# Kernel optimization log

Measured on AMD Instinct MI355X. Metric: run time of the kernel, lower is better.

Reference implementation:

```python
import jax, jax.numpy as jnp
from jax import lax
import numpy as np

H = 64  # hiddenSize
I = 9   # inputSize

def _init_lstm_params(key, in_dim, hidden):
    k = 1.0 / np.sqrt(hidden)
    ks = jax.random.split(key, 4)
    w_ih = jax.random.uniform(ks[0], (4 * hidden, in_dim), minval=-k, maxval=k, dtype=jnp.float32)
    w_hh = jax.random.uniform(ks[1], (4 * hidden, hidden), minval=-k, maxval=k, dtype=jnp.float32)
    b_ih = jax.random.uniform(ks[2], (4 * hidden,), minval=-k, maxval=k, dtype=jnp.float32)
    b_hh = jax.random.uniform(ks[3], (4 * hidden,), minval=-k, maxval=k, dtype=jnp.float32)
    return w_ih, w_hh, b_ih, b_hh

def setup_inputs() -> dict:
    key = jax.random.key(0)
    kx, k0, k1, kl = jax.random.split(key, 4)
    x = jax.random.normal(kx, (4096, 336, I), dtype=jnp.float32)
    w_ih0, w_hh0, b_ih0, b_hh0 = _init_lstm_params(k0, I, H)
    w_ih1, w_hh1, b_ih1, b_hh1 = _init_lstm_params(k1, H, H)
    klw, klb = jax.random.split(kl)
    k = 1.0 / np.sqrt(H)
    w_lin = jax.random.uniform(klw, (1, H), minval=-k, maxval=k, dtype=jnp.float32)
    b_lin = jax.random.uniform(klb, (1,), minval=-k, maxval=k, dtype=jnp.float32)
    return {"x": x, "w_ih0": w_ih0, "w_hh0": w_hh0, "b_ih0": b_ih0, "b_hh0": b_hh0,
            "w_ih1": w_ih1, "w_hh1": w_hh1, "b_ih1": b_ih1, "b_hh1": b_hh1,
            "w_lin": w_lin, "b_lin": b_lin}

def _lstm_layer(x_seq, w_ih, w_hh, b_ih, b_hh):
    # x_seq: [B, T, D] -> hidden sequence [B, T, H]. PyTorch gate order: i, f, g, o.
    B = x_seq.shape[0]
    hidden = w_hh.shape[1]
    # Precompute input contribution for all timesteps in one GEMM.
    pre = jnp.einsum('btd,gd->btg', x_seq, w_ih) + b_ih + b_hh  # [B, T, 4H]
    pre_t = jnp.swapaxes(pre, 0, 1)  # [T, B, 4H]

    def step(carry, p):
        h, c = carry
        gates = p + h @ w_hh.T  # [B, 4H]
        i, f, g, o = jnp.split(gates, 4, axis=-1)
        i = jax.nn.sigmoid(i)
        f = jax.nn.sigmoid(f)
        g = jnp.tanh(g)
        o = jax.nn.sigmoid(o)
        c = f * c + i * g
        h = o * jnp.tanh(c)
        return (h, c), h

    h0 = jnp.zeros((B, hidden), dtype=x_seq.dtype)
    c0 = jnp.zeros((B, hidden), dtype=x_seq.dtype)
    _, hs = lax.scan(step, (h0, c0), pre_t)
    return jnp.swapaxes(hs, 0, 1)  # [B, T, H]

def reference(x, w_ih0, w_hh0, b_ih0, b_hh0, w_ih1, w_hh1, b_ih1, b_hh1, w_lin, b_lin):
    h1 = _lstm_layer(x, w_ih0, w_hh0, b_ih0, b_hh0)     # layer 1 (dropout inactive in eval)
    h2 = _lstm_layer(h1, w_ih1, w_hh1, b_ih1, b_hh1)    # layer 2
    last = h2[:, -1, :]                                  # [B, H]
    out = jax.nn.sigmoid(last @ w_lin.T + b_lin)         # [B, 1]
    return out
```

## Files before the change

### kernel.cpp

```cpp
#include <hip/hip_runtime.h>
#include <hip/hip_bf16.h>
#include <stdint.h>


typedef __attribute__((ext_vector_type(8))) short s16x8;
typedef __attribute__((ext_vector_type(4))) short s16x4;
typedef __attribute__((ext_vector_type(4))) float f32x4;

#define MFMA_BF16 __builtin_amdgcn_mfma_f32_16x16x32_bf16

__device__ __forceinline__ short f2bf(float f) {
    uint32_t u = __builtin_bit_cast(uint32_t, f);
    u += 0x7fffu + ((u >> 16) & 1u);
    return (short)(u >> 16);
}

__device__ __forceinline__ s16x4 pack_bf16x4(float a, float b, float c, float d) {
    union { uint32_t u[2]; s16x4 s; } r;
    asm("v_cvt_pk_bf16_f32 %0, %1, %2" : "=v"(r.u[0]) : "v"(a), "v"(b));
    asm("v_cvt_pk_bf16_f32 %0, %1, %2" : "=v"(r.u[1]) : "v"(c), "v"(d));
    return r.s;
}

__device__ __forceinline__ float fsigm(float x) {
    float e = __builtin_amdgcn_exp2f(x * -1.4426950408889634f);
    return __builtin_amdgcn_rcpf(1.0f + e);
}
__device__ __forceinline__ float ftanh(float x) {
    float e = __builtin_amdgcn_exp2f(x * 2.8853900817779268f);
    return 1.0f - 2.0f * __builtin_amdgcn_rcpf(1.0f + e);
}

__global__ __launch_bounds__(512, 1)
void lstm_fused(const float* __restrict__ x,
                const float* __restrict__ w_ih0, const float* __restrict__ w_hh0,
                const float* __restrict__ b_ih0, const float* __restrict__ b_hh0,
                const float* __restrict__ w_ih1, const float* __restrict__ w_hh1,
                const float* __restrict__ b_ih1, const float* __restrict__ b_hh1,
                const float* __restrict__ w_lin, const float* __restrict__ b_lin,
                float* __restrict__ out)
{
    __shared__ __align__(16) short xs[16 * 512];
    __shared__ __align__(16) short h0s[2][16 * 64];
    __shared__ __align__(16) short h1s[2][16 * 64];
    __shared__ float red[4][16];

    const int tid  = threadIdx.x;
    const int w    = tid >> 6;
    const int role = w >> 2;
    const int wl   = w & 3;
    const int l    = tid & 63;
    const int bcol = l & 15;
    const int q    = l >> 4;
    const int b0   = blockIdx.x * 16;

    for (int i = tid; i < 16 * 512; i += 512) xs[i] = 0;
    for (int i = tid; i < 16 * 64; i += 512) {
        h0s[0][i] = 0; h0s[1][i] = 0; h1s[0][i] = 0; h1s[1][i] = 0;
    }
    __syncthreads();

    s16x8 aW[4][4];
    f32x4 bias[4];
    #pragma unroll
    for (int m = 0; m < 4; ++m) {
        const int R = m * 64 + wl * 16 + bcol;
        if (role == 0) {
            #pragma unroll
            for (int r = 0; r < 8; ++r) {
                int k = q * 8 + r;
                aW[m][0][r] = (k < 9) ? f2bf(w_ih0[R * 9 + k]) : (short)0;
            }
            #pragma unroll
            for (int kf = 0; kf < 2; ++kf) {
                const float* p = w_hh0 + R * 64 + kf * 32 + q * 8;
                #pragma unroll
                for (int r = 0; r < 8; ++r) aW[m][1 + kf][r] = f2bf(p[r]);
            }
            #pragma unroll
            for (int r = 0; r < 8; ++r) aW[m][3][r] = 0;
            #pragma unroll
            for (int r = 0; r < 4; ++r) {
                int G = m * 64 + wl * 16 + q * 4 + r;
                bias[m][r] = b_ih0[G] + b_hh0[G];
            }
        } else {
            #pragma unroll
            for (int kf = 0; kf < 4; ++kf) {
                int ks = kf * 32 + q * 8;
                const float* p = (ks < 64) ? (w_ih1 + R * 64 + ks)
                                           : (w_hh1 + R * 64 + (ks - 64));
                #pragma unroll
                for (int r = 0; r < 8; ++r) aW[m][kf][r] = f2bf(p[r]);
            }
            #pragma unroll
            for (int r = 0; r < 4; ++r) {
                int G = m * 64 + wl * 16 + q * 4 + r;
                bias[m][r] = b_ih1[G] + b_hh1[G];
            }
        }
    }

    f32x4 c = {0.f, 0.f, 0.f, 0.f};
    f32x4 hq = {0.f, 0.f, 0.f, 0.f};

    const int hrd0 = bcol * 64 + (((q    ) ^ (bcol & 7)) << 3);
    const int hrd1 = bcol * 64 + (((4 + q) ^ (bcol & 7)) << 3);
    const int hwr  = bcol * 64 + (((wl * 2 + (q >> 1)) ^ (bcol & 7)) << 3)
                   + ((q & 1) << 2);
    const int xrd  = bcol * 32 + ((q ^ (bcol & 3)) << 3);

    const int    ld_b = (tid & 255) >> 4, ld_t = tid & 15;
    const float* xrow = x + (size_t)(b0 + ld_b) * (336 * 9) + ld_t * 9;
    const int    xs_wr_base = ld_t * 512 + ld_b * 32;
    const int    xswzw = (ld_b & 3) << 3;

    #pragma unroll 1
    for (int i = 0; i <= 336; ++i) {
        if ((i & 15) == 0 && i < 336) {
            if (tid < 256) {
                const float* xp = xrow + (size_t)i * 9;
                #pragma unroll
                for (int d = 0; d < 9; ++d)
                    xs[(xs_wr_base + d) ^ xswzw] = f2bf(xp[d]);
            }
            __syncthreads();
        }

        const short* h0r = h0s[(i & 1) ^ 1];
        const short* h1r = h1s[(i & 1) ^ 1];
        short*       h0w = h0s[i & 1];
        short*       h1w = h1s[i & 1];

        const bool act0 = (role == 0) & (i < 336);
        const bool act1 = (role == 1) & (i > 0);

        if (act0) {
            s16x8 bx = *(const s16x8*)&xs[(i & 15) * 512 + xrd];
            s16x8 ba = *(const s16x8*)&h0r[hrd0];
            s16x8 bb = *(const s16x8*)&h0r[hrd1];
            f32x4 acc[4];
            #pragma unroll
            for (int m = 0; m < 4; ++m) acc[m] = MFMA_BF16(aW[m][0], bx, bias[m], 0, 0, 0);
            #pragma unroll
            for (int m = 0; m < 4; ++m) acc[m] = MFMA_BF16(aW[m][1], ba, acc[m], 0, 0, 0);
            #pragma unroll
            for (int m = 0; m < 4; ++m) acc[m] = MFMA_BF16(aW[m][2], bb, acc[m], 0, 0, 0);
            #pragma unroll
            for (int r = 0; r < 4; ++r) {
                float iv = fsigm(acc[0][r]);
                float fv = fsigm(acc[1][r]);
                float gv = ftanh(acc[2][r]);
                float ov = fsigm(acc[3][r]);
                float cc = fv * c[r] + iv * gv;
                c[r] = cc;
                hq[r] = ov * ftanh(cc);
            }
            *(s16x4*)&h0w[hwr] = pack_bf16x4(hq[0], hq[1], hq[2], hq[3]);
        } else if (act1) {
            s16x8 ba  = *(const s16x8*)&h0r[hrd0];
            s16x8 bb  = *(const s16x8*)&h0r[hrd1];
            s16x8 b1a = *(const s16x8*)&h1r[hrd0];
            s16x8 b1b = *(const s16x8*)&h1r[hrd1];
            f32x4 acc[4];
            #pragma unroll
            for (int m = 0; m < 4; ++m) acc[m] = MFMA_BF16(aW[m][0], ba,  bias[m], 0, 0, 0);
            #pragma unroll
            for (int m = 0; m < 4; ++m) acc[m] = MFMA_BF16(aW[m][1], bb,  acc[m], 0, 0, 0);
            #pragma unroll
            for (int m = 0; m < 4; ++m) acc[m] = MFMA_BF16(aW[m][2], b1a, acc[m], 0, 0, 0);
            #pragma unroll
            for (int m = 0; m < 4; ++m) acc[m] = MFMA_BF16(aW[m][3], b1b, acc[m], 0, 0, 0);
            #pragma unroll
            for (int r = 0; r < 4; ++r) {
                float iv = fsigm(acc[0][r]);
                float fv = fsigm(acc[1][r]);
                float gv = ftanh(acc[2][r]);
                float ov = fsigm(acc[3][r]);
                float cc = fv * c[r] + iv * gv;
                c[r] = cc;
                hq[r] = ov * ftanh(cc);
            }
            *(s16x4*)&h1w[hwr] = pack_bf16x4(hq[0], hq[1], hq[2], hq[3]);
        }

        __syncthreads();
    }

    if (role == 1) {
        float part = hq[0] * w_lin[wl * 16 + q * 4 + 0]
                   + hq[1] * w_lin[wl * 16 + q * 4 + 1]
                   + hq[2] * w_lin[wl * 16 + q * 4 + 2]
                   + hq[3] * w_lin[wl * 16 + q * 4 + 3];
        part += __shfl_xor(part, 16, 64);
        part += __shfl_xor(part, 32, 64);
        if (q == 0) red[wl][bcol] = part;
    }
    __syncthreads();
    if (tid < 16) {
        float s = red[0][tid] + red[1][tid] + red[2][tid] + red[3][tid] + b_lin[0];
        out[b0 + tid] = fsigm(s);
    }
}

extern "C" void kernel_launch(void* const* d_in, const int* in_sizes, int n_in,
                              void* d_out, int out_size, void* d_ws, size_t ws_size,
                              hipStream_t stream) {
    const float* x     = (const float*)d_in[0];
    const float* w_ih0 = (const float*)d_in[1];
    const float* w_hh0 = (const float*)d_in[2];
    const float* b_ih0 = (const float*)d_in[3];
    const float* b_hh0 = (const float*)d_in[4];
    const float* w_ih1 = (const float*)d_in[5];
    const float* w_hh1 = (const float*)d_in[6];
    const float* b_ih1 = (const float*)d_in[7];
    const float* b_hh1 = (const float*)d_in[8];
    const float* w_lin = (const float*)d_in[9];
    const float* b_lin = (const float*)d_in[10];

    lstm_fused<<<dim3(256), dim3(512), 0, stream>>>(
        x, w_ih0, w_hh0, b_ih0, b_hh0,
        w_ih1, w_hh1, b_ih1, b_hh1,
        w_lin, b_lin, (float*)d_out);
}
```

Baseline: 306.1 us.

## Split each step into two phases so layer-0 MFMA overlaps layer-1 activations

Each timestep is restructured into two barrier-separated phases. In one phase layer-0 waves run their MFMAs while layer-1 waves evaluate activations from the previous step's accumulators, and in the other phase the roles swap. The aim is to keep the matrix unit and the vector ALU busy at the same time instead of one after the other, at the cost of two barriers per step and one extra loop iteration. Separately, the exp2 scale factors are folded into the bf16 weights and biases so the activations skip one multiply each, which changes rounding slightly. The layer-1 h buffer also drops to a single copy.

```diff
diff --git a/kernel.cpp b/kernel.cpp
--- a/kernel.cpp
+++ b/kernel.cpp
@@ -8,6 +8,8 @@
 typedef __attribute__((ext_vector_type(4))) float f32x4;
 
 #define MFMA_BF16 __builtin_amdgcn_mfma_f32_16x16x32_bf16
+#define LOG2E     1.4426950408889634f
+#define TWO_LOG2E 2.8853900817779268f
 
 __device__ __forceinline__ short f2bf(float f) {
     uint32_t u = __builtin_bit_cast(uint32_t, f);
@@ -22,13 +24,8 @@
     return r.s;
 }
 
-__device__ __forceinline__ float fsigm(float x) {
-    float e = __builtin_amdgcn_exp2f(x * -1.4426950408889634f);
-    return __builtin_amdgcn_rcpf(1.0f + e);
-}
-__device__ __forceinline__ float ftanh(float x) {
-    float e = __builtin_amdgcn_exp2f(x * 2.8853900817779268f);
-    return 1.0f - 2.0f * __builtin_amdgcn_rcpf(1.0f + e);
+__device__ __forceinline__ float rcp1p2(float t) {
+    return __builtin_amdgcn_rcpf(1.0f + __builtin_amdgcn_exp2f(t));
 }
 
 __global__ __launch_bounds__(512, 1)
@@ -42,7 +39,7 @@
 {
     __shared__ __align__(16) short xs[16 * 512];
     __shared__ __align__(16) short h0s[2][16 * 64];
-    __shared__ __align__(16) short h1s[2][16 * 64];
+    __shared__ __align__(16) short h1s[16 * 64];
     __shared__ float red[4][16];
 
     const int tid  = threadIdx.x;
@@ -56,33 +53,36 @@
 
     for (int i = tid; i < 16 * 512; i += 512) xs[i] = 0;
     for (int i = tid; i < 16 * 64; i += 512) {
-        h0s[0][i] = 0; h0s[1][i] = 0; h1s[0][i] = 0; h1s[1][i] = 0;
+        h0s[0][i] = 0; h0s[1][i] = 0; h1s[i] = 0;
     }
     __syncthreads();
+
+    const float scm[4] = { -LOG2E, -LOG2E, TWO_LOG2E, -LOG2E };
 
     s16x8 aW[4][4];
     f32x4 bias[4];
     #pragma unroll
     for (int m = 0; m < 4; ++m) {
         const int R = m * 64 + wl * 16 + bcol;
+        const float sc = scm[m];
         if (role == 0) {
             #pragma unroll
             for (int r = 0; r < 8; ++r) {
                 int k = q * 8 + r;
-                aW[m][0][r] = (k < 9) ? f2bf(w_ih0[R * 9 + k]) : (short)0;
+                aW[m][0][r] = (k < 9) ? f2bf(w_ih0[R * 9 + k] * sc) : (short)0;
             }
             #pragma unroll
             for (int kf = 0; kf < 2; ++kf) {
                 const float* p = w_hh0 + R * 64 + kf * 32 + q * 8;
                 #pragma unroll
-                for (int r = 0; r < 8; ++r) aW[m][1 + kf][r] = f2bf(p[r]);
+                for (int r = 0; r < 8; ++r) aW[m][1 + kf][r] = f2bf(p[r] * sc);
             }
             #pragma unroll
             for (int r = 0; r < 8; ++r) aW[m][3][r] = 0;
             #pragma unroll
             for (int r = 0; r < 4; ++r) {
                 int G = m * 64 + wl * 16 + q * 4 + r;
-                bias[m][r] = b_ih0[G] + b_hh0[G];
+                bias[m][r] = (b_ih0[G] + b_hh0[G]) * sc;
             }
         } else {
             #pragma unroll
@@ -91,18 +91,21 @@
                 const float* p = (ks < 64) ? (w_ih1 + R * 64 + ks)
                                            : (w_hh1 + R * 64 + (ks - 64));
                 #pragma unroll
-                for (int r = 0; r < 8; ++r) aW[m][kf][r] = f2bf(p[r]);
+                for (int r = 0; r < 8; ++r) aW[m][kf][r] = f2bf(p[r] * sc);
             }
             #pragma unroll
             for (int r = 0; r < 4; ++r) {
                 int G = m * 64 + wl * 16 + q * 4 + r;
-                bias[m][r] = b_ih1[G] + b_hh1[G];
-            }
-        }
-    }
-
-    f32x4 c = {0.f, 0.f, 0.f, 0.f};
+                bias[m][r] = (b_ih1[G] + b_hh1[G]) * sc;
+            }
+        }
+    }
+
+    f32x4 c  = {0.f, 0.f, 0.f, 0.f};
     f32x4 hq = {0.f, 0.f, 0.f, 0.f};
+    f32x4 accL1[4];
+    #pragma unroll
+    for (int m = 0; m < 4; ++m) accL1[m] = (f32x4){0.f, 0.f, 0.f, 0.f};
 
     const int hrd0 = bcol * 64 + (((q    ) ^ (bcol & 7)) << 3);
     const int hrd1 = bcol * 64 + (((4 + q) ^ (bcol & 7)) << 3);
@@ -116,7 +119,7 @@
     const int    xswzw = (ld_b & 3) << 3;
 
     #pragma unroll 1
-    for (int i = 0; i <= 336; ++i) {
+    for (int i = 0; i <= 337; ++i) {
         if ((i & 15) == 0 && i < 336) {
             if (tid < 256) {
                 const float* xp = xrow + (size_t)i * 9;
@@ -127,63 +130,69 @@
             __syncthreads();
         }
 
-        const short* h0r = h0s[(i & 1) ^ 1];
-        const short* h1r = h1s[(i & 1) ^ 1];
-        short*       h0w = h0s[i & 1];
-        short*       h1w = h1s[i & 1];
-
-        const bool act0 = (role == 0) & (i < 336);
-        const bool act1 = (role == 1) & (i > 0);
-
-        if (act0) {
-            s16x8 bx = *(const s16x8*)&xs[(i & 15) * 512 + xrd];
-            s16x8 ba = *(const s16x8*)&h0r[hrd0];
-            s16x8 bb = *(const s16x8*)&h0r[hrd1];
-            f32x4 acc[4];
-            #pragma unroll
-            for (int m = 0; m < 4; ++m) acc[m] = MFMA_BF16(aW[m][0], bx, bias[m], 0, 0, 0);
-            #pragma unroll
-            for (int m = 0; m < 4; ++m) acc[m] = MFMA_BF16(aW[m][1], ba, acc[m], 0, 0, 0);
-            #pragma unroll
-            for (int m = 0; m < 4; ++m) acc[m] = MFMA_BF16(aW[m][2], bb, acc[m], 0, 0, 0);
-            #pragma unroll
-            for (int r = 0; r < 4; ++r) {
-                float iv = fsigm(acc[0][r]);
-                float fv = fsigm(acc[1][r]);
-                float gv = ftanh(acc[2][r]);
-                float ov = fsigm(acc[3][r]);
-                float cc = fv * c[r] + iv * gv;
-                c[r] = cc;
-                hq[r] = ov * ftanh(cc);
-            }
-            *(s16x4*)&h0w[hwr] = pack_bf16x4(hq[0], hq[1], hq[2], hq[3]);
-        } else if (act1) {
-            s16x8 ba  = *(const s16x8*)&h0r[hrd0];
-            s16x8 bb  = *(const s16x8*)&h0r[hrd1];
-            s16x8 b1a = *(const s16x8*)&h1r[hrd0];
-            s16x8 b1b = *(const s16x8*)&h1r[hrd1];
-            f32x4 acc[4];
-            #pragma unroll
-            for (int m = 0; m < 4; ++m) acc[m] = MFMA_BF16(aW[m][0], ba,  bias[m], 0, 0, 0);
-            #pragma unroll
-            for (int m = 0; m < 4; ++m) acc[m] = MFMA_BF16(aW[m][1], bb,  acc[m], 0, 0, 0);
-            #pragma unroll
-            for (int m = 0; m < 4; ++m) acc[m] = MFMA_BF16(aW[m][2], b1a, acc[m], 0, 0, 0);
-            #pragma unroll
-            for (int m = 0; m < 4; ++m) acc[m] = MFMA_BF16(aW[m][3], b1b, acc[m], 0, 0, 0);
-            #pragma unroll
-            for (int r = 0; r < 4; ++r) {
-                float iv = fsigm(acc[0][r]);
-                float fv = fsigm(acc[1][r]);
-                float gv = ftanh(acc[2][r]);
-                float ov = fsigm(acc[3][r]);
-                float cc = fv * c[r] + iv * gv;
-                c[r] = cc;
-                hq[r] = ov * ftanh(cc);
-            }
-            *(s16x4*)&h1w[hwr] = pack_bf16x4(hq[0], hq[1], hq[2], hq[3]);
-        }
-
+        f32x4 acc0[4];
+        if (role == 0) {
+            if (i <= 335) {
+                s16x8 bx = *(const s16x8*)&xs[(i & 15) * 512 + xrd];
+                const short* h0r = h0s[(i & 1) ^ 1];
+                s16x8 ba = *(const s16x8*)&h0r[hrd0];
+                s16x8 bb = *(const s16x8*)&h0r[hrd1];
+                #pragma unroll
+                for (int m = 0; m < 4; ++m) acc0[m] = MFMA_BF16(aW[m][0], bx, bias[m], 0, 0, 0);
+                #pragma unroll
+                for (int m = 0; m < 4; ++m) acc0[m] = MFMA_BF16(aW[m][1], ba, acc0[m], 0, 0, 0);
+                #pragma unroll
+                for (int m = 0; m < 4; ++m) acc0[m] = MFMA_BF16(aW[m][2], bb, acc0[m], 0, 0, 0);
+            }
+        } else {
+            if (i >= 2) {
+                #pragma unroll
+                for (int r = 0; r < 4; ++r) {
+                    float iv = rcp1p2(accL1[0][r]);
+                    float fv = rcp1p2(accL1[1][r]);
+                    float gv = fmaf(-2.f, rcp1p2(accL1[2][r]), 1.f);
+                    float ov = rcp1p2(accL1[3][r]);
+                    float cc = fv * c[r] + iv * gv;
+                    c[r] = cc;
+                    hq[r] = ov * fmaf(-2.f, rcp1p2(cc * TWO_LOG2E), 1.f);
+                }
+                *(s16x4*)&h1s[hwr] = pack_bf16x4(hq[0], hq[1], hq[2], hq[3]);
+            }
+        }
+        __syncthreads();
+
+        if (role == 0) {
+            if (i <= 335) {
+                #pragma unroll
+                for (int r = 0; r < 4; ++r) {
+                    float iv = rcp1p2(acc0[0][r]);
+                    float fv = rcp1p2(acc0[1][r]);
+                    float gv = fmaf(-2.f, rcp1p2(acc0[2][r]), 1.f);
+                    float ov = rcp1p2(acc0[3][r]);
+                    float cc = fv * c[r] + iv * gv;
+                    c[r] = cc;
+                    hq[r] = ov * fmaf(-2.f, rcp1p2(cc * TWO_LOG2E), 1.f);
+                }
+                short* h0w = h0s[i & 1];
+                *(s16x4*)&h0w[hwr] = pack_bf16x4(hq[0], hq[1], hq[2], hq[3]);
+            }
+        } else {
+            if (i >= 1 && i <= 336) {
+                const short* h0r = h0s[(i & 1) ^ 1];
+                s16x8 ba  = *(const s16x8*)&h0r[hrd0];
+                s16x8 bb  = *(const s16x8*)&h0r[hrd1];
+                s16x8 b1a = *(const s16x8*)&h1s[hrd0];
+                s16x8 b1b = *(const s16x8*)&h1s[hrd1];
+                #pragma unroll
+                for (int m = 0; m < 4; ++m) accL1[m] = MFMA_BF16(aW[m][0], ba,  bias[m], 0, 0, 0);
+                #pragma unroll
+                for (int m = 0; m < 4; ++m) accL1[m] = MFMA_BF16(aW[m][1], bb,  accL1[m], 0, 0, 0);
+                #pragma unroll
+                for (int m = 0; m < 4; ++m) accL1[m] = MFMA_BF16(aW[m][2], b1a, accL1[m], 0, 0, 0);
+                #pragma unroll
+                for (int m = 0; m < 4; ++m) accL1[m] = MFMA_BF16(aW[m][3], b1b, accL1[m], 0, 0, 0);
+            }
+        }
         __syncthreads();
     }
 
@@ -199,7 +208,7 @@
     __syncthreads();
     if (tid < 16) {
         float s = red[0][tid] + red[1][tid] + red[2][tid] + red[3][tid] + b_lin[0];
-        out[b0 + tid] = fsigm(s);
+        out[b0 + tid] = rcp1p2(-s * LOG2E);
     }
 }
 
```

Result: no change. 301.2 us (-1.6%).
